# Optimization experiments

Hardware: AMD Instinct MI355X
Metric: run time of the kernel (lower is better)

The kernel has to match this reference:

```python
import jax, jax.numpy as jnp
import numpy as np

B_BATCH = 2048
D = 1024
L_CACHE = 3
N_LAYERS = 12
LAYER_IDX = 0


def setup_inputs() -> dict:
    key = jax.random.key(0)
    ks = jax.random.split(key, 5)
    x = jax.random.normal(ks[0], (B_BATCH, 1, D), dtype=jnp.float32)
    conv_cache = jax.random.normal(ks[1], (N_LAYERS, B_BATCH, D, L_CACHE), dtype=jnp.float32)
    cache_position = jnp.ones((1,), dtype=jnp.int64 if jax.config.jax_enable_x64 else jnp.int32)
    in_proj_w = jax.random.normal(ks[2], (3 * D, D), dtype=jnp.float32) * 0.02
    out_proj_w = jax.random.normal(ks[3], (D, D), dtype=jnp.float32) * 0.02
    conv_w = jax.random.normal(ks[4], (D, 1, L_CACHE), dtype=jnp.float32) * 0.2
    return {"x": x, "conv_cache": conv_cache, "cache_position": cache_position,
            "in_proj_w": in_proj_w, "out_proj_w": out_proj_w, "conv_w": conv_w}


def reference(x, conv_cache, cache_position, in_proj_w, out_proj_w, conv_w):
    # x: [B, 1, D] decode step. attention_mask path is a no-op for seq_len==1.
    # in_proj then transpose(-1,-2): [B, 3D, 1]
    BCx = jnp.swapaxes(jnp.einsum('bld,ed->ble', x, in_proj_w), -1, -2)
    Bg, Cg, xg = jnp.split(BCx, 3, axis=-2)  # each [B, D, 1]
    Bx = Bg * xg  # gate; feeds (discarded) cache update in the original

    # WithCache branch (cache_position[0] > 0):
    conv_state = conv_cache[LAYER_IDX]  # [B, D, L_cache]
    # Original computes new_conv_state = roll + indexed write of Bx, but it is
    # discarded; conv_out uses the OLD conv_state. Faithfully reproduced:
    # new_conv_state = jnp.roll(conv_state, -1, axis=-1).at[:, :, jnp.clip(cache_position, 0, L_CACHE-1)].set(Bx)
    conv_out = jnp.sum(conv_state * conv_w[:, 0, :], axis=-1)[..., None]  # [B, D, 1]

    y = Cg * conv_out                      # [B, D, 1]
    y = jnp.swapaxes(y, -1, -2)            # [B, 1, D]
    return jnp.einsum('bld,ed->ble', y, out_proj_w)
```

## Files before the change

kernel.cpp:

```cpp
#include <hip/hip_runtime.h>
#include <hip/hip_bf16.h>


#define MDIM 2048
#define NDIM 1024
#define KDIM 1024

typedef __attribute__((ext_vector_type(8))) short bf16x8;
typedef __attribute__((ext_vector_type(4))) float f32x4;

__device__ __forceinline__ unsigned short bf16rn(float f) {
    unsigned int u = __builtin_bit_cast(unsigned int, f);
    return (unsigned short)((u + 0x7FFFu + ((u >> 16) & 1u)) >> 16);
}

#define GLDS16(gp, lp)                                                          \
    __builtin_amdgcn_global_load_lds(                                           \
        (const __attribute__((address_space(1))) void*)(gp),                    \
        (__attribute__((address_space(3))) void*)(lp), 16, 0, 0)

__global__ __launch_bounds__(256) void prep_cast(
    const float* __restrict__ x, const float* __restrict__ w1,
    const float* __restrict__ w2, unsigned short* __restrict__ xb,
    unsigned short* __restrict__ w1b, unsigned short* __restrict__ w2b)
{
    const int t = blockIdx.x * 256 + threadIdx.x;
    const int X4 = MDIM * KDIM / 4;
    const int W4 = KDIM * NDIM / 4;
    float4 v;
    unsigned short* dst;
    if (t < X4) {
        v = ((const float4*)x)[t];
        dst = xb + (size_t)t * 4;
    } else if (t < X4 + W4) {
        int u = t - X4;
        v = ((const float4*)(w1 + (size_t)NDIM * KDIM))[u];
        dst = w1b + (size_t)u * 4;
    } else {
        int u = t - X4 - W4;
        v = ((const float4*)w2)[u];
        dst = w2b + (size_t)u * 4;
    }
    ushort4 o;
    o.x = bf16rn(v.x); o.y = bf16rn(v.y); o.z = bf16rn(v.z); o.w = bf16rn(v.w);
    *(ushort4*)dst = o;
}

template <bool GATE>
__global__ __launch_bounds__(128) void gemm(
    const unsigned short* __restrict__ A, const unsigned short* __restrict__ Bm,
    const float* __restrict__ cache,
    const float* __restrict__ convw,
    unsigned short* __restrict__ Ybf, float* __restrict__ Yout)
{
    __shared__ unsigned short ldsA[64 * 64];
    __shared__ unsigned short ldsB[64 * 64];

    const int tid  = threadIdx.x;
    const int lane = tid & 63;
    const int w    = tid >> 6;
    const int col  = lane & 15;
    const int quad = lane >> 4;
    const int m0   = blockIdx.y * 64;
    const int n0   = blockIdx.x * 64;

    const int rsub = lane >> 3;
    const int kg   = (lane & 7) ^ rsub;
    size_t aoff[4], boff[4];
#pragma unroll
    for (int t = 0; t < 4; ++t) {
        const int c = 4 * w + t;
        aoff[t] = (size_t)(m0 + 8 * c + rsub) * KDIM + kg * 8;
        boff[t] = (size_t)(n0 + 8 * c + rsub) * KDIM + kg * 8;
    }

    f32x4 acc[4][2] = {};

    for (int k0 = 0; k0 < KDIM; k0 += 64) {
#pragma unroll
        for (int t = 0; t < 4; ++t) {
            const int c = 4 * w + t;
            GLDS16(A + aoff[t] + k0, &ldsA[c * 512]);
            GLDS16(Bm + boff[t] + k0, &ldsB[c * 512]);
        }
        __syncthreads();

#pragma unroll
        for (int ks = 0; ks < 2; ++ks) {
            const int slot = (ks * 4 + quad) ^ (col & 7);
            bf16x8 av[4], bv[2];
#pragma unroll
            for (int i = 0; i < 4; ++i)
                av[i] = *(const bf16x8*)&ldsA[(i * 16 + col) * 64 + slot * 8];
#pragma unroll
            for (int j = 0; j < 2; ++j)
                bv[j] = *(const bf16x8*)&ldsB[(w * 32 + j * 16 + col) * 64 + slot * 8];
#pragma unroll
            for (int i = 0; i < 4; ++i)
#pragma unroll
                for (int j = 0; j < 2; ++j)
                    acc[i][j] = __builtin_amdgcn_mfma_f32_16x16x32_bf16(
                        av[i], bv[j], acc[i][j], 0, 0, 0);
        }
        __syncthreads();
    }

#pragma unroll
    for (int j = 0; j < 2; ++j) {
        const int n = n0 + w * 32 + j * 16 + col;
        float cw0, cw1, cw2;
        if (GATE) {
            cw0 = convw[n * 3 + 0];
            cw1 = convw[n * 3 + 1];
            cw2 = convw[n * 3 + 2];
        }
#pragma unroll
        for (int i = 0; i < 4; ++i) {
#pragma unroll
            for (int r = 0; r < 4; ++r) {
                const int m = m0 + i * 16 + quad * 4 + r;
                float v = acc[i][j][r];
                if (GATE) {
                    const float* cp = cache + ((size_t)m * NDIM + n) * 3;
                    v *= cp[0] * cw0 + cp[1] * cw1 + cp[2] * cw2;
                    Ybf[(size_t)m * NDIM + n] = bf16rn(v);
                } else {
                    Yout[(size_t)m * NDIM + n] = v;
                }
            }
        }
    }
}

extern "C" void kernel_launch(void* const* d_in, const int* in_sizes, int n_in,
                              void* d_out, int out_size, void* d_ws, size_t ws_size,
                              hipStream_t stream)
{
    const float* x     = (const float*)d_in[0];
    const float* cache = (const float*)d_in[1];
    const float* w1    = (const float*)d_in[3];
    const float* w2    = (const float*)d_in[4];
    const float* cw    = (const float*)d_in[5];
    float* out = (float*)d_out;

    unsigned short* xb  = (unsigned short*)d_ws;
    unsigned short* w1b = xb  + (size_t)MDIM * KDIM;
    unsigned short* w2b = w1b + (size_t)KDIM * NDIM;
    unsigned short* yb  = w2b + (size_t)KDIM * NDIM;

    prep_cast<<<dim3(4096), dim3(256), 0, stream>>>(x, w1, w2, xb, w1b, w2b);

    dim3 grid(NDIM / 64, MDIM / 64);
    gemm<true><<<grid, dim3(128), 0, stream>>>(xb, w1b, cache, cw, yb, nullptr);
    gemm<false><<<grid, dim3(128), 0, stream>>>(yb, w2b, nullptr, nullptr, nullptr, out);
}
```

Measured before the change: 378.5 us.

## Fuse fp32-to-bf16 cast into GEMM tile loads with double-buffered LDS

Removes the separate prep_cast kernel. Each GEMM now reads fp32 operands straight from global memory, converts them to bf16 in registers with v_cvt_pk_bf16_f32, and writes them into swizzled LDS. LDS is double-buffered so the next tile's global loads are issued before the current tile's MFMAs. This saves one launch and a round trip through workspace memory, at the cost of more register pressure and re-reading fp32 weights once per block row instead of once overall.

```diff
diff --git a/kernel.cpp b/kernel.cpp
--- a/kernel.cpp
+++ b/kernel.cpp
@@ -1,5 +1,4 @@
 #include <hip/hip_runtime.h>
-#include <hip/hip_bf16.h>
 
 
 #define MDIM 2048
@@ -14,47 +13,26 @@
     return (unsigned short)((u + 0x7FFFu + ((u >> 16) & 1u)) >> 16);
 }
 
+__device__ __forceinline__ unsigned int cvtpk(float lo, float hi) {
+    unsigned int r;
+    asm("v_cvt_pk_bf16_f32 %0, %1, %2" : "=v"(r) : "v"(lo), "v"(hi));
+    return r;
+}
+
 #define GLDS16(gp, lp)                                                          \
     __builtin_amdgcn_global_load_lds(                                           \
         (const __attribute__((address_space(1))) void*)(gp),                    \
         (__attribute__((address_space(3))) void*)(lp), 16, 0, 0)
 
-__global__ __launch_bounds__(256) void prep_cast(
-    const float* __restrict__ x, const float* __restrict__ w1,
-    const float* __restrict__ w2, unsigned short* __restrict__ xb,
-    unsigned short* __restrict__ w1b, unsigned short* __restrict__ w2b)
-{
-    const int t = blockIdx.x * 256 + threadIdx.x;
-    const int X4 = MDIM * KDIM / 4;
-    const int W4 = KDIM * NDIM / 4;
-    float4 v;
-    unsigned short* dst;
-    if (t < X4) {
-        v = ((const float4*)x)[t];
-        dst = xb + (size_t)t * 4;
-    } else if (t < X4 + W4) {
-        int u = t - X4;
-        v = ((const float4*)(w1 + (size_t)NDIM * KDIM))[u];
-        dst = w1b + (size_t)u * 4;
-    } else {
-        int u = t - X4 - W4;
-        v = ((const float4*)w2)[u];
-        dst = w2b + (size_t)u * 4;
-    }
-    ushort4 o;
-    o.x = bf16rn(v.x); o.y = bf16rn(v.y); o.z = bf16rn(v.z); o.w = bf16rn(v.w);
-    *(ushort4*)dst = o;
-}
-
 template <bool GATE>
 __global__ __launch_bounds__(128) void gemm(
-    const unsigned short* __restrict__ A, const unsigned short* __restrict__ Bm,
+    const void* __restrict__ Aptr, const float* __restrict__ Bw,
     const float* __restrict__ cache,
     const float* __restrict__ convw,
     unsigned short* __restrict__ Ybf, float* __restrict__ Yout)
 {
-    __shared__ unsigned short ldsA[64 * 64];
-    __shared__ unsigned short ldsB[64 * 64];
+    __shared__ __align__(16) unsigned short ldsA[2][64 * 64];
+    __shared__ __align__(16) unsigned short ldsB[2][64 * 64];
 
     const int tid  = threadIdx.x;
     const int lane = tid & 63;
@@ -64,26 +42,76 @@
     const int m0   = blockIdx.y * 64;
     const int n0   = blockIdx.x * 64;
 
-    const int rsub = lane >> 3;
-    const int kg   = (lane & 7) ^ rsub;
-    size_t aoff[4], boff[4];
+    const int r = tid >> 1;
+    const int h = tid & 1;
+
+    const float4* bsrc = (const float4*)(Bw + (size_t)(n0 + r) * KDIM + h * 32);
+    const float4* asrc = nullptr;
+    size_t aoff[4] = {};
+    if constexpr (GATE) {
+        asrc = (const float4*)((const float*)Aptr + (size_t)(m0 + r) * KDIM + h * 32);
+    } else {
+        const int rsub = lane >> 3;
+        const int kg   = (lane & 7) ^ rsub;
 #pragma unroll
-    for (int t = 0; t < 4; ++t) {
-        const int c = 4 * w + t;
-        aoff[t] = (size_t)(m0 + 8 * c + rsub) * KDIM + kg * 8;
-        boff[t] = (size_t)(n0 + 8 * c + rsub) * KDIM + kg * 8;
+        for (int t = 0; t < 4; ++t) {
+            const int c = 4 * w + t;
+            aoff[t] = (size_t)(m0 + 8 * c + rsub) * KDIM + kg * 8;
+        }
     }
+
+    float4 a4[8], b4[8];
+
+    auto load_tiles = [&](int k0, int buf) {
+        const int kf = k0 >> 2;
+        if constexpr (GATE) {
+#pragma unroll
+            for (int j = 0; j < 8; ++j) a4[j] = asrc[kf + j];
+        } else {
+#pragma unroll
+            for (int t = 0; t < 4; ++t)
+                GLDS16((const unsigned short*)Aptr + aoff[t] + k0,
+                       &ldsA[buf][(4 * w + t) * 512]);
+        }
+#pragma unroll
+        for (int j = 0; j < 8; ++j) b4[j] = bsrc[kf + j];
+    };
+
+    auto cvt_write = [&](int buf) {
+#pragma unroll
+        for (int g = 0; g < 4; ++g) {
+            uint4 wv;
+            wv.x = cvtpk(b4[2 * g].x, b4[2 * g].y);
+            wv.y = cvtpk(b4[2 * g].z, b4[2 * g].w);
+            wv.z = cvtpk(b4[2 * g + 1].x, b4[2 * g + 1].y);
+            wv.w = cvtpk(b4[2 * g + 1].z, b4[2 * g + 1].w);
+            const int slot = (4 * h + g) ^ (r & 7);
+            *(uint4*)&ldsB[buf][r * 64 + slot * 8] = wv;
+        }
+        if constexpr (GATE) {
+#pragma unroll
+            for (int g = 0; g < 4; ++g) {
+                uint4 wv;
+                wv.x = cvtpk(a4[2 * g].x, a4[2 * g].y);
+                wv.y = cvtpk(a4[2 * g].z, a4[2 * g].w);
+                wv.z = cvtpk(a4[2 * g + 1].x, a4[2 * g + 1].y);
+                wv.w = cvtpk(a4[2 * g + 1].z, a4[2 * g + 1].w);
+                const int slot = (4 * h + g) ^ (r & 7);
+                *(uint4*)&ldsA[buf][r * 64 + slot * 8] = wv;
+            }
+        }
+    };
 
     f32x4 acc[4][2] = {};
 
+    load_tiles(0, 0);
+    cvt_write(0);
+    __syncthreads();
+
+    int cur = 0;
     for (int k0 = 0; k0 < KDIM; k0 += 64) {
-#pragma unroll
-        for (int t = 0; t < 4; ++t) {
-            const int c = 4 * w + t;
-            GLDS16(A + aoff[t] + k0, &ldsA[c * 512]);
-            GLDS16(Bm + boff[t] + k0, &ldsB[c * 512]);
-        }
-        __syncthreads();
+        const bool more = (k0 + 64 < KDIM);
+        if (more) load_tiles(k0 + 64, cur ^ 1);
 
 #pragma unroll
         for (int ks = 0; ks < 2; ++ks) {
@@ -91,10 +119,10 @@
             bf16x8 av[4], bv[2];
 #pragma unroll
             for (int i = 0; i < 4; ++i)
-                av[i] = *(const bf16x8*)&ldsA[(i * 16 + col) * 64 + slot * 8];
+                av[i] = *(const bf16x8*)&ldsA[cur][(i * 16 + col) * 64 + slot * 8];
 #pragma unroll
             for (int j = 0; j < 2; ++j)
-                bv[j] = *(const bf16x8*)&ldsB[(w * 32 + j * 16 + col) * 64 + slot * 8];
+                bv[j] = *(const bf16x8*)&ldsB[cur][(w * 32 + j * 16 + col) * 64 + slot * 8];
 #pragma unroll
             for (int i = 0; i < 4; ++i)
 #pragma unroll
@@ -102,14 +130,19 @@
                     acc[i][j] = __builtin_amdgcn_mfma_f32_16x16x32_bf16(
                         av[i], bv[j], acc[i][j], 0, 0, 0);
         }
-        __syncthreads();
+
+        if (more) {
+            cvt_write(cur ^ 1);
+            __syncthreads();
+            cur ^= 1;
+        }
     }
 
 #pragma unroll
     for (int j = 0; j < 2; ++j) {
         const int n = n0 + w * 32 + j * 16 + col;
-        float cw0, cw1, cw2;
-        if (GATE) {
+        float cw0 = 0.f, cw1 = 0.f, cw2 = 0.f;
+        if constexpr (GATE) {
             cw0 = convw[n * 3 + 0];
             cw1 = convw[n * 3 + 1];
             cw2 = convw[n * 3 + 2];
@@ -117,10 +150,10 @@
 #pragma unroll
         for (int i = 0; i < 4; ++i) {
 #pragma unroll
-            for (int r = 0; r < 4; ++r) {
-                const int m = m0 + i * 16 + quad * 4 + r;
-                float v = acc[i][j][r];
-                if (GATE) {
+            for (int rr = 0; rr < 4; ++rr) {
+                const int m = m0 + i * 16 + quad * 4 + rr;
+                float v = acc[i][j][rr];
+                if constexpr (GATE) {
                     const float* cp = cache + ((size_t)m * NDIM + n) * 3;
                     v *= cp[0] * cw0 + cp[1] * cw1 + cp[2] * cw2;
                     Ybf[(size_t)m * NDIM + n] = bf16rn(v);
@@ -143,14 +176,12 @@
     const float* cw    = (const float*)d_in[5];
     float* out = (float*)d_out;
 
-    unsigned short* xb  = (unsigned short*)d_ws;
-    unsigned short* w1b = xb  + (size_t)MDIM * KDIM;
-    unsigned short* w2b = w1b + (size_t)KDIM * NDIM;
-    unsigned short* yb  = w2b + (size_t)KDIM * NDIM;
-
-    prep_cast<<<dim3(4096), dim3(256), 0, stream>>>(x, w1, w2, xb, w1b, w2b);
+    unsigned short* yb = (unsigned short*)d_ws;
 
     dim3 grid(NDIM / 64, MDIM / 64);
-    gemm<true><<<grid, dim3(128), 0, stream>>>(xb, w1b, cache, cw, yb, nullptr);
-    gemm<false><<<grid, dim3(128), 0, stream>>>(yb, w2b, nullptr, nullptr, nullptr, out);
+    gemm<true><<<grid, dim3(128), 0, stream>>>(
+        x, w1 + (size_t)NDIM * KDIM,
+        cache, cw, yb, nullptr);
+    gemm<false><<<grid, dim3(128), 0, stream>>>(
+        yb, w2, nullptr, nullptr, nullptr, out);
 }
```

Result: slower. 418.9 us (+10.7%).

## Triple-buffer LDS tiles with async global-to-LDS prefetch in GEMM

Applied to the files above, without the earlier changes.

Replaces the single-buffered load/sync/compute loop with a three-stage LDS ring. Tiles two steps ahead are issued via global_load_lds while the current tile is computed. Manual vmcnt waits and one barrier per iteration replace the two __syncthreads, so memory latency can overlap with MFMA work. LDS use triples to 48KB per block, which may reduce occupancy, and correctness now depends on the hand-counted vmcnt values.

```diff
diff --git a/kernel.cpp b/kernel.cpp
--- a/kernel.cpp
+++ b/kernel.cpp
@@ -1,5 +1,4 @@
 #include <hip/hip_runtime.h>
-#include <hip/hip_bf16.h>
 
 
 #define MDIM 2048
@@ -53,8 +52,8 @@
     const float* __restrict__ convw,
     unsigned short* __restrict__ Ybf, float* __restrict__ Yout)
 {
-    __shared__ unsigned short ldsA[64 * 64];
-    __shared__ unsigned short ldsB[64 * 64];
+    __shared__ __align__(16) unsigned short ldsA[3][64 * 64];
+    __shared__ __align__(16) unsigned short ldsB[3][64 * 64];
 
     const int tid  = threadIdx.x;
     const int lane = tid & 63;
@@ -74,16 +73,26 @@
         boff[t] = (size_t)(n0 + 8 * c + rsub) * KDIM + kg * 8;
     }
 
-    f32x4 acc[4][2] = {};
-
-    for (int k0 = 0; k0 < KDIM; k0 += 64) {
+    auto stage = [&](int tt, int buf) {
 #pragma unroll
         for (int t = 0; t < 4; ++t) {
             const int c = 4 * w + t;
-            GLDS16(A + aoff[t] + k0, &ldsA[c * 512]);
-            GLDS16(Bm + boff[t] + k0, &ldsB[c * 512]);
+            GLDS16(A  + aoff[t] + tt * 64, &ldsA[buf][c * 512]);
+            GLDS16(Bm + boff[t] + tt * 64, &ldsB[buf][c * 512]);
         }
-        __syncthreads();
+    };
+
+    f32x4 acc[4][2] = {};
+
+    stage(0, 0);
+    stage(1, 1);
+    asm volatile("s_waitcnt vmcnt(8)" ::: "memory");
+    __builtin_amdgcn_s_barrier();
+    __builtin_amdgcn_sched_barrier(0);
+
+    int cur = 0;
+    for (int t = 0; t < 16; ++t) {
+        if (t < 14) stage(t + 2, (t + 2) % 3);
 
 #pragma unroll
         for (int ks = 0; ks < 2; ++ks) {
@@ -91,10 +100,10 @@
             bf16x8 av[4], bv[2];
 #pragma unroll
             for (int i = 0; i < 4; ++i)
-                av[i] = *(const bf16x8*)&ldsA[(i * 16 + col) * 64 + slot * 8];
+                av[i] = *(const bf16x8*)&ldsA[cur][(i * 16 + col) * 64 + slot * 8];
 #pragma unroll
             for (int j = 0; j < 2; ++j)
-                bv[j] = *(const bf16x8*)&ldsB[(w * 32 + j * 16 + col) * 64 + slot * 8];
+                bv[j] = *(const bf16x8*)&ldsB[cur][(w * 32 + j * 16 + col) * 64 + slot * 8];
 #pragma unroll
             for (int i = 0; i < 4; ++i)
 #pragma unroll
@@ -102,13 +111,22 @@
                     acc[i][j] = __builtin_amdgcn_mfma_f32_16x16x32_bf16(
                         av[i], bv[j], acc[i][j], 0, 0, 0);
         }
-        __syncthreads();
+
+        if (t < 15) {
+            if (t < 14)
+                asm volatile("s_waitcnt vmcnt(8) lgkmcnt(0)" ::: "memory");
+            else
+                asm volatile("s_waitcnt vmcnt(0) lgkmcnt(0)" ::: "memory");
+            __builtin_amdgcn_s_barrier();
+            __builtin_amdgcn_sched_barrier(0);
+        }
+        cur = (cur == 2) ? 0 : cur + 1;
     }
 
 #pragma unroll
     for (int j = 0; j < 2; ++j) {
         const int n = n0 + w * 32 + j * 16 + col;
-        float cw0, cw1, cw2;
+        float cw0 = 0.f, cw1 = 0.f, cw2 = 0.f;
         if (GATE) {
             cw0 = convw[n * 3 + 0];
             cw1 = convw[n * 3 + 1];
@@ -117,9 +135,9 @@
 #pragma unroll
         for (int i = 0; i < 4; ++i) {
 #pragma unroll
-            for (int r = 0; r < 4; ++r) {
-                const int m = m0 + i * 16 + quad * 4 + r;
-                float v = acc[i][j][r];
+            for (int rr = 0; rr < 4; ++rr) {
+                const int m = m0 + i * 16 + quad * 4 + rr;
+                float v = acc[i][j][rr];
                 if (GATE) {
                     const float* cp = cache + ((size_t)m * NDIM + n) * 3;
                     v *= cp[0] * cw0 + cp[1] * cw1 + cp[2] * cw2;
```

Result: no change. 380.0 us (+0.4%).
